# Kernel optimization log

Hardware: AMD Instinct MI355X
Metric: run time of the kernel (lower is better)

The kernel has to match this reference:

```python
import jax, jax.numpy as jnp
import numpy as np

B, S, C, H, EPS = 8, 1024, 768, 12, 1e-6
D = C // H            # head dim 64
F_HID = int(C * 4.0)  # 3072


def _layer_norm(x, w, b):
    mu = jnp.mean(x, axis=-1, keepdims=True)
    var = jnp.mean(jnp.square(x - mu), axis=-1, keepdims=True)
    return (x - mu) * jax.lax.rsqrt(var + EPS) * w + b


def setup_inputs() -> dict:
    key = jax.random.key(0)
    ks = jax.random.split(key, 16)
    sc_c = 1.0 / np.sqrt(C)
    sc_f = 1.0 / np.sqrt(F_HID)
    return {
        "hidden_states": jax.random.normal(ks[0], (B, S, C), jnp.float32),
        "ln1_w": jnp.ones((C,), jnp.float32),
        "ln1_b": jnp.zeros((C,), jnp.float32),
        # weights stored [in, out] (transpose of torch Linear layout; same math)
        "q_w": jax.random.normal(ks[1], (C, C), jnp.float32) * sc_c,
        "q_b": jnp.zeros((C,), jnp.float32),
        "k_w": jax.random.normal(ks[2], (C, C), jnp.float32) * sc_c,
        "k_b": jnp.zeros((C,), jnp.float32),
        "v_w": jax.random.normal(ks[3], (C, C), jnp.float32) * sc_c,
        "v_b": jnp.zeros((C,), jnp.float32),
        "o_w": jax.random.normal(ks[4], (C, C), jnp.float32) * sc_c,
        "o_b": jnp.zeros((C,), jnp.float32),
        "lam1": jnp.ones((C,), jnp.float32),
        "ln2_w": jnp.ones((C,), jnp.float32),
        "ln2_b": jnp.zeros((C,), jnp.float32),
        "fc1_w": jax.random.normal(ks[5], (C, F_HID), jnp.float32) * sc_c,
        "fc1_b": jnp.zeros((F_HID,), jnp.float32),
        "fc2_w": jax.random.normal(ks[6], (F_HID, C), jnp.float32) * sc_f,
        "fc2_b": jnp.zeros((C,), jnp.float32),
    }


def reference(hidden_states, ln1_w, ln1_b, q_w, q_b, k_w, k_b, v_w, v_b,
              o_w, o_b, lam1, ln2_w, ln2_b, fc1_w, fc1_b, fc2_w, fc2_b):
    shortcut = hidden_states
    x = _layer_norm(hidden_states, ln1_w, ln1_b)
    # QKV projections, split heads: [B,S,C] -> [B,H,S,D]
    def heads(t):
        return t.reshape(B, S, H, D).transpose(0, 2, 1, 3)
    q = heads(x @ q_w + q_b)
    k = heads(x @ k_w + k_b)
    v = heads(x @ v_w + v_b)
    scores = jnp.einsum("bhsd,bhtd->bhst", q, k) / np.sqrt(D)
    probs = jax.nn.softmax(scores, axis=-1)  # dropout p=0 -> identity
    ctx = jnp.einsum("bhst,bhtd->bhsd", probs, v)
    ctx = ctx.transpose(0, 2, 1, 3).reshape(B, S, C)
    attn_out = ctx @ o_w + o_b
    hidden = attn_out * lam1 + shortcut
    y = _layer_norm(hidden, ln2_w, ln2_b)
    y = jax.nn.gelu(y @ fc1_w + fc1_b, approximate=False)
    y = y @ fc2_w + fc2_b
    return y * lam2_mul(lam1) + hidden if False else (y * jnp.ones_like(lam1) * lam1 * 0 + y) * 0 + y * lam1 * 0 + (y * _LAM2 + hidden)


# NOTE: layer_scale2 has its own parameter; expose it cleanly instead of the hack above.
_LAM2 = None

def lam2_mul(x):
    return x

# Clean final definitions (override the above):

def setup_inputs() -> dict:  # noqa: F811
    key = jax.random.key(0)
    ks = jax.random.split(key, 16)
    sc_c = 1.0 / np.sqrt(C)
    sc_f = 1.0 / np.sqrt(F_HID)
    return {
        "hidden_states": jax.random.normal(ks[0], (B, S, C), jnp.float32),
        "ln1_w": jnp.ones((C,), jnp.float32),
        "ln1_b": jnp.zeros((C,), jnp.float32),
        "q_w": jax.random.normal(ks[1], (C, C), jnp.float32) * sc_c,
        "q_b": jnp.zeros((C,), jnp.float32),
        "k_w": jax.random.normal(ks[2], (C, C), jnp.float32) * sc_c,
        "k_b": jnp.zeros((C,), jnp.float32),
        "v_w": jax.random.normal(ks[3], (C, C), jnp.float32) * sc_c,
        "v_b": jnp.zeros((C,), jnp.float32),
        "o_w": jax.random.normal(ks[4], (C, C), jnp.float32) * sc_c,
        "o_b": jnp.zeros((C,), jnp.float32),
        "lam1": jnp.ones((C,), jnp.float32),
        "ln2_w": jnp.ones((C,), jnp.float32),
        "ln2_b": jnp.zeros((C,), jnp.float32),
        "fc1_w": jax.random.normal(ks[5], (C, F_HID), jnp.float32) * sc_c,
        "fc1_b": jnp.zeros((F_HID,), jnp.float32),
        "fc2_w": jax.random.normal(ks[6], (F_HID, C), jnp.float32) * sc_f,
        "fc2_b": jnp.zeros((C,), jnp.float32),
        "lam2": jnp.ones((C,), jnp.float32),
    }


def reference(hidden_states, ln1_w, ln1_b, q_w, q_b, k_w, k_b, v_w, v_b,  # noqa: F811
              o_w, o_b, lam1, ln2_w, ln2_b, fc1_w, fc1_b, fc2_w, fc2_b, lam2):
    shortcut = hidden_states
    x = _layer_norm(hidden_states, ln1_w, ln1_b)
    def heads(t):
        return t.reshape(B, S, H, D).transpose(0, 2, 1, 3)  # [B,H,S,D]
    q = heads(x @ q_w + q_b)
    k = heads(x @ k_w + k_b)
    v = heads(x @ v_w + v_b)
    scores = jnp.einsum("bhsd,bhtd->bhst", q, k) / np.sqrt(D)
    probs = jax.nn.softmax(scores, axis=-1)  # attn dropout p=0 (eval)
    ctx = jnp.einsum("bhst,bhtd->bhsd", probs, v)
    ctx = ctx.transpose(0, 2, 1, 3).reshape(B, S, C)
    attn_out = ctx @ o_w + o_b            # SelfOutput dense (dropout p=0)
    hidden = attn_out * lam1 + shortcut   # layer_scale1 + residual
    y = _layer_norm(hidden, ln2_w, ln2_b)
    y = jax.nn.gelu(y @ fc1_w + fc1_b, approximate=False)  # nn.GELU exact
    y = y @ fc2_w + fc2_b
    return y * lam2 + hidden              # layer_scale2 + residual
```

## Files before the change

kernel.cpp:

```cpp
#include <hip/hip_runtime.h>
#include <stdint.h>
#include <stddef.h>

using bf16x8 = __attribute__((ext_vector_type(8))) short;
using f32x4  = __attribute__((ext_vector_type(4))) float;

#define DEV static __device__ __forceinline__

DEV unsigned short f2bf(float f) {
  union { float f; uint32_t u; } x; x.f = f;
  uint32_t u = x.u;
  u += 0x7fffu + ((u >> 16) & 1u);
  return (unsigned short)(u >> 16);
}

DEV void gld_lds16(const void* g, void* lds) {
  __builtin_amdgcn_global_load_lds(
      (__attribute__((address_space(1))) void*)(uintptr_t)g,
      (__attribute__((address_space(3))) void*)(uintptr_t)lds, 16, 0, 0);
}

__global__ void transpose_w(const float* __restrict__ in, unsigned short* __restrict__ out,
                            int K, int N) {
  __shared__ float tile[64][65];
  int n0 = blockIdx.x * 64, k0 = blockIdx.y * 64;
  int tx = threadIdx.x & 15, ty = threadIdx.x >> 4;
#pragma unroll
  for (int j = 0; j < 4; ++j) {
    int r = ty + j * 16;
    float4 v = *(const float4*)(in + (size_t)(k0 + r) * N + n0 + tx * 4);
    tile[r][tx * 4 + 0] = v.x; tile[r][tx * 4 + 1] = v.y;
    tile[r][tx * 4 + 2] = v.z; tile[r][tx * 4 + 3] = v.w;
  }
  __syncthreads();
#pragma unroll
  for (int j = 0; j < 4; ++j) {
    int n = ty + j * 16;
    ushort4 o;
    o.x = f2bf(tile[tx * 4 + 0][n]);
    o.y = f2bf(tile[tx * 4 + 1][n]);
    o.z = f2bf(tile[tx * 4 + 2][n]);
    o.w = f2bf(tile[tx * 4 + 3][n]);
    *(ushort4*)(out + (size_t)(n0 + n) * K + k0 + tx * 4) = o;
  }
}

__global__ void pack_bias(const float* __restrict__ q, const float* __restrict__ k,
                          const float* __restrict__ v, float* __restrict__ out) {
  int i = blockIdx.x * 256 + threadIdx.x;
  const float* s = (i < 768) ? q : ((i < 1536) ? k : v);
  int r = i; if (r >= 1536) r -= 1536; else if (r >= 768) r -= 768;
  out[i] = s[r];
}

__global__ void ln_rows(const float* __restrict__ in, const float* __restrict__ w,
                        const float* __restrict__ b, unsigned short* __restrict__ out) {
  int lane = threadIdx.x & 63;
  int row = blockIdx.x * 4 + (threadIdx.x >> 6);
  const float* p = in + (size_t)row * 768;
  float4 v[3];
  float s = 0.f, s2 = 0.f;
#pragma unroll
  for (int j = 0; j < 3; ++j) {
    v[j] = *(const float4*)(p + j * 256 + lane * 4);
    s  += v[j].x + v[j].y + v[j].z + v[j].w;
    s2 += v[j].x * v[j].x + v[j].y * v[j].y + v[j].z * v[j].z + v[j].w * v[j].w;
  }
#pragma unroll
  for (int o = 32; o >= 1; o >>= 1) { s += __shfl_xor(s, o); s2 += __shfl_xor(s2, o); }
  float mu = s * (1.f / 768.f);
  float var = s2 * (1.f / 768.f) - mu * mu;
  float rs = rsqrtf(var + 1e-6f);
#pragma unroll
  for (int j = 0; j < 3; ++j) {
    int c = j * 256 + lane * 4;
    float4 wv = *(const float4*)(w + c);
    float4 bv = *(const float4*)(b + c);
    ushort4 o4;
    o4.x = f2bf((v[j].x - mu) * rs * wv.x + bv.x);
    o4.y = f2bf((v[j].y - mu) * rs * wv.y + bv.y);
    o4.z = f2bf((v[j].z - mu) * rs * wv.z + bv.z);
    o4.w = f2bf((v[j].w - mu) * rs * wv.w + bv.w);
    *(ushort4*)(out + (size_t)row * 768 + c) = o4;
  }
}

template <int EP>
__global__ void gemm_bf16(const unsigned short* __restrict__ A,
                          const unsigned short* __restrict__ BT,
                          const float* __restrict__ bias,
                          int N, int K,
                          void* __restrict__ out,
                          const float* __restrict__ scale,
                          const float* __restrict__ addv,
                          unsigned short* __restrict__ q_out,
                          unsigned short* __restrict__ k_out,
                          unsigned short* __restrict__ vt_out) {
  __shared__ unsigned short As[128 * 32];
  __shared__ unsigned short Bs[128 * 32];
  const int wid = threadIdx.x >> 6, lane = threadIdx.x & 63;
  const int bm = blockIdx.y * 128, bn = blockIdx.x * 128;
  const int wr = wid >> 1, wc = wid & 1;
  f32x4 acc[4][4] = {};

  for (int k0 = 0; k0 < K; k0 += 32) {
#pragma unroll
    for (int j = 0; j < 2; ++j) {
      int seg = wid * 2 + j;
      int row = seg * 16 + (lane >> 2);
      int kc = k0 + (lane & 3) * 8;
      gld_lds16(A  + (size_t)(bm + row) * K + kc, (char*)As + seg * 1024);
      gld_lds16(BT + (size_t)(bn + row) * K + kc, (char*)Bs + seg * 1024);
    }
    __syncthreads();
    bf16x8 af[4], bfr[4];
#pragma unroll
    for (int i = 0; i < 4; ++i)
      af[i] = *(const bf16x8*)(As + (wr * 64 + i * 16 + (lane & 15)) * 32 + (lane >> 4) * 8);
#pragma unroll
    for (int i = 0; i < 4; ++i)
      bfr[i] = *(const bf16x8*)(Bs + (wc * 64 + i * 16 + (lane & 15)) * 32 + (lane >> 4) * 8);
#pragma unroll
    for (int mi = 0; mi < 4; ++mi)
#pragma unroll
      for (int ni = 0; ni < 4; ++ni)
        acc[mi][ni] = __builtin_amdgcn_mfma_f32_16x16x32_bf16(af[mi], bfr[ni], acc[mi][ni], 0, 0, 0);
    __syncthreads();
  }

#pragma unroll
  for (int mi = 0; mi < 4; ++mi) {
#pragma unroll
    for (int ni = 0; ni < 4; ++ni) {
      int col = bn + wc * 64 + ni * 16 + (lane & 15);
      float bcol = bias[col];
#pragma unroll
      for (int r = 0; r < 4; ++r) {
        int row = bm + wr * 64 + mi * 16 + (lane >> 4) * 4 + r;
        float v = acc[mi][ni][r] + bcol;
        if (EP == 0) {
          int b = row >> 10, s = row & 1023;
          int piece = col / 768;
          int rc = col - piece * 768;
          int h = rc >> 6, d = rc & 63;
          unsigned short bvv = f2bf(v);
          if (piece == 0)      q_out [((size_t)(b * 12 + h) * 1024 + s) * 64 + d] = bvv;
          else if (piece == 1) k_out [((size_t)(b * 12 + h) * 1024 + s) * 64 + d] = bvv;
          else                 vt_out[((size_t)(b * 12 + h) * 64 + d) * 1024 + s] = bvv;
        } else if (EP == 1) {
          ((float*)out)[(size_t)row * 768 + col] = v * scale[col] + addv[(size_t)row * 768 + col];
        } else if (EP == 2) {
          float g = 0.5f * v * (1.f + erff(v * 0.70710678118654752f));
          ((unsigned short*)out)[(size_t)row * (size_t)N + col] = f2bf(g);
        } else {
          ((float*)out)[(size_t)row * 768 + col] = v * scale[col] + addv[(size_t)row * 768 + col];
        }
      }
    }
  }
}

__global__ __launch_bounds__(512) void attn_fwd(const unsigned short* __restrict__ qb,
                         const unsigned short* __restrict__ kb,
                         const unsigned short* __restrict__ vtb,
                         unsigned short* __restrict__ ctx) {
  __shared__ unsigned short Ks[64 * 64];
  __shared__ unsigned short VTs[64 * 64];
  __shared__ unsigned short Ps[8][16 * 64];
  const int wid = threadIdx.x >> 6, lane = threadIdx.x & 63;
  const int wg = (blockIdx.x & 7) * 96 + (blockIdx.x >> 3);
  const int bh = wg >> 3;
  const int qt = wg & 7;
  const int q0 = qt * 128 + wid * 16;
  const unsigned short* qh  = qb  + (size_t)bh * 1024 * 64;
  const unsigned short* kh  = kb  + (size_t)bh * 1024 * 64;
  const unsigned short* vth = vtb + (size_t)bh * 64 * 1024;

  bf16x8 qf[2];
#pragma unroll
  for (int kk = 0; kk < 2; ++kk)
    qf[kk] = *(const bf16x8*)(qh + (size_t)(q0 + (lane & 15)) * 64 + kk * 32 + (lane >> 4) * 8);

  bf16x8 ones;
#pragma unroll
  for (int i = 0; i < 8; ++i) ones[i] = (short)0x3F80;

  f32x4 o_acc[4] = {};
  float m_run[4], l_run[4];
#pragma unroll
  for (int r = 0; r < 4; ++r) { m_run[r] = -INFINITY; l_run[r] = 0.f; }
  const float sc = 0.125f * 1.44269504088896f;

  const int srow = threadIdx.x >> 3;
  const int sbc  = ((threadIdx.x & 7) * 16) ^ ((srow & 7) << 4);
  const int scol = (threadIdx.x & 7) * 8;

  for (int s0 = 0; s0 < 1024; s0 += 64) {
    *(uint4*)((char*)Ks  + srow * 128 + sbc) = *(const uint4*)(kh  + (size_t)(s0 + srow) * 64 + scol);
    *(uint4*)((char*)VTs + srow * 128 + sbc) = *(const uint4*)(vth + (size_t)srow * 1024 + s0 + scol);
    __syncthreads();

    f32x4 s_acc[4] = {};
#pragma unroll
    for (int kk = 0; kk < 2; ++kk) {
#pragma unroll
      for (int nt = 0; nt < 4; ++nt) {
        int row = nt * 16 + (lane & 15);
        int off = (kk * 64 + (lane >> 4) * 16) ^ ((row & 7) << 4);
        bf16x8 kf = *(const bf16x8*)((const char*)Ks + row * 128 + off);
        s_acc[nt] = __builtin_amdgcn_mfma_f32_16x16x32_bf16(qf[kk], kf, s_acc[nt], 0, 0, 0);
      }
    }
    float mt[4];
#pragma unroll
    for (int r = 0; r < 4; ++r) {
      float mm = fmaxf(fmaxf(s_acc[0][r], s_acc[1][r]), fmaxf(s_acc[2][r], s_acc[3][r]));
#pragma unroll
      for (int o = 8; o >= 1; o >>= 1) mm = fmaxf(mm, __shfl_xor(mm, o, 16));
      mt[r] = mm * sc;
    }
    bool need = (mt[0] > m_run[0] + 8.f) | (mt[1] > m_run[1] + 8.f) |
                (mt[2] > m_run[2] + 8.f) | (mt[3] > m_run[3] + 8.f);
    if (__ballot(need)) {
      float alpha[4];
#pragma unroll
      for (int r = 0; r < 4; ++r) {
        float mn = fmaxf(m_run[r], mt[r]);
        alpha[r] = exp2f(m_run[r] - mn);
        m_run[r] = mn;
        l_run[r] *= alpha[r];
      }
#pragma unroll
      for (int dt = 0; dt < 4; ++dt)
#pragma unroll
        for (int r = 0; r < 4; ++r)
          o_acc[dt][r] = o_acc[dt][r] * alpha[r];
    }
    unsigned short* pw = Ps[wid];
#pragma unroll
    for (int nt = 0; nt < 4; ++nt)
#pragma unroll
      for (int r = 0; r < 4; ++r) {
        float p = exp2f(s_acc[nt][r] * sc - m_run[r]);
        int qrow = (lane >> 4) * 4 + r;
        int bc = (nt * 16 + (lane & 15)) * 2;
        *(unsigned short*)((char*)pw + qrow * 128 + (bc ^ ((qrow & 7) << 4))) = f2bf(p);
      }
    asm volatile("s_waitcnt lgkmcnt(0)" ::: "memory");
    f32x4 lacc = {};
#pragma unroll
    for (int kk = 0; kk < 2; ++kk) {
      int prow = lane & 15;
      int poff = (kk * 64 + (lane >> 4) * 16) ^ ((prow & 7) << 4);
      bf16x8 pf = *(const bf16x8*)((const char*)pw + prow * 128 + poff);
      lacc = __builtin_amdgcn_mfma_f32_16x16x32_bf16(pf, ones, lacc, 0, 0, 0);
#pragma unroll
      for (int dt = 0; dt < 4; ++dt) {
        int vrow = dt * 16 + (lane & 15);
        int voff = (kk * 64 + (lane >> 4) * 16) ^ ((vrow & 7) << 4);
        bf16x8 vf = *(const bf16x8*)((const char*)VTs + vrow * 128 + voff);
        o_acc[dt] = __builtin_amdgcn_mfma_f32_16x16x32_bf16(pf, vf, o_acc[dt], 0, 0, 0);
      }
    }
#pragma unroll
    for (int r = 0; r < 4; ++r) l_run[r] += lacc[r];
    __syncthreads();
  }

  int b = bh / 12, h = bh % 12;
#pragma unroll
  for (int r = 0; r < 4; ++r) {
    float inv = 1.f / l_run[r];
    int sr = q0 + (lane >> 4) * 4 + r;
#pragma unroll
    for (int dt = 0; dt < 4; ++dt)
      ctx[((size_t)(b * 1024 + sr)) * 768 + h * 64 + dt * 16 + (lane & 15)] =
          f2bf(o_acc[dt][r] * inv);
  }
}

extern "C" void kernel_launch(void* const* d_in, const int* in_sizes, int n_in,
                              void* d_out, int out_size, void* d_ws, size_t ws_size,
                              hipStream_t stream) {
  const float* hs    = (const float*)d_in[0];
  const float* ln1_w = (const float*)d_in[1];
  const float* ln1_b = (const float*)d_in[2];
  const float* q_w   = (const float*)d_in[3];
  const float* q_b   = (const float*)d_in[4];
  const float* k_w   = (const float*)d_in[5];
  const float* k_b   = (const float*)d_in[6];
  const float* v_w   = (const float*)d_in[7];
  const float* v_b   = (const float*)d_in[8];
  const float* o_w   = (const float*)d_in[9];
  const float* o_b   = (const float*)d_in[10];
  const float* lam1  = (const float*)d_in[11];
  const float* ln2_w = (const float*)d_in[12];
  const float* ln2_b = (const float*)d_in[13];
  const float* fc1_w = (const float*)d_in[14];
  const float* fc1_b = (const float*)d_in[15];
  const float* fc2_w = (const float*)d_in[16];
  const float* fc2_b = (const float*)d_in[17];
  const float* lam2  = (const float*)d_in[18];

  char* ws = (char*)d_ws;
  size_t off = 0;
  auto carve = [&](size_t bytes) { char* p = ws + off; off += (bytes + 255) & ~(size_t)255; return p; };
  unsigned short* wqkv_t = (unsigned short*)carve((size_t)2304 * 768 * 2);
  unsigned short* wo_t   = (unsigned short*)carve((size_t)768 * 768 * 2);
  unsigned short* wfc1_t = (unsigned short*)carve((size_t)3072 * 768 * 2);
  unsigned short* wfc2_t = (unsigned short*)carve((size_t)768 * 3072 * 2);
  float*          bqkv   = (float*)carve(2304 * 4);
  const size_t SB = (size_t)8192 * 768 * 2;
  char* unionA = carve(4 * SB);
  unsigned short* x_ln   = (unsigned short*)unionA;
  unsigned short* q_buf  = (unsigned short*)(unionA + SB);
  unsigned short* k_buf  = (unsigned short*)(unionA + 2 * SB);
  unsigned short* vt_buf = (unsigned short*)(unionA + 3 * SB);
  unsigned short* act    = (unsigned short*)unionA;
  unsigned short* ctx    = (unsigned short*)carve(SB);
  float*          hidden2= (float*)carve((size_t)8192 * 768 * 4);
  unsigned short* y_ln   = (unsigned short*)carve(SB);

  pack_bias<<<dim3(9), dim3(256), 0, stream>>>(q_b, k_b, v_b, bqkv);
  transpose_w<<<dim3(12, 12), dim3(256), 0, stream>>>(q_w, wqkv_t, 768, 768);
  transpose_w<<<dim3(12, 12), dim3(256), 0, stream>>>(k_w, wqkv_t + (size_t)768 * 768, 768, 768);
  transpose_w<<<dim3(12, 12), dim3(256), 0, stream>>>(v_w, wqkv_t + (size_t)2 * 768 * 768, 768, 768);
  transpose_w<<<dim3(12, 12), dim3(256), 0, stream>>>(o_w, wo_t, 768, 768);
  transpose_w<<<dim3(48, 12), dim3(256), 0, stream>>>(fc1_w, wfc1_t, 768, 3072);
  transpose_w<<<dim3(12, 48), dim3(256), 0, stream>>>(fc2_w, wfc2_t, 3072, 768);

  ln_rows<<<dim3(2048), dim3(256), 0, stream>>>(hs, ln1_w, ln1_b, x_ln);
  gemm_bf16<0><<<dim3(18, 64), dim3(256), 0, stream>>>(x_ln, wqkv_t, bqkv, 2304, 768,
      nullptr, nullptr, nullptr, q_buf, k_buf, vt_buf);
  attn_fwd<<<dim3(768), dim3(512), 0, stream>>>(q_buf, k_buf, vt_buf, ctx);
  gemm_bf16<1><<<dim3(6, 64), dim3(256), 0, stream>>>(ctx, wo_t, o_b, 768, 768,
      hidden2, lam1, hs, nullptr, nullptr, nullptr);
  ln_rows<<<dim3(2048), dim3(256), 0, stream>>>(hidden2, ln2_w, ln2_b, y_ln);
  gemm_bf16<2><<<dim3(24, 64), dim3(256), 0, stream>>>(y_ln, wfc1_t, fc1_b, 3072, 768,
      act, nullptr, nullptr, nullptr, nullptr, nullptr);
  gemm_bf16<3><<<dim3(6, 64), dim3(256), 0, stream>>>(act, wfc2_t, fc2_b, 768, 3072,
      d_out, lam2, hidden2, nullptr, nullptr, nullptr);
}
```

Measured before the change: 471.0 us.

## Rewrite attention with 32x32 MFMA, register-resident P, and double-buffered K/V

```diff
diff --git a/kernel.cpp b/kernel.cpp
--- a/kernel.cpp
+++ b/kernel.cpp
@@ -1,9 +1,11 @@
 #include <hip/hip_runtime.h>
+#include <hip/hip_bf16.h>
 #include <stdint.h>
 #include <stddef.h>
 
 using bf16x8 = __attribute__((ext_vector_type(8))) short;
 using f32x4  = __attribute__((ext_vector_type(4))) float;
+using f32x16 = __attribute__((ext_vector_type(16))) float;
 
 #define DEV static __device__ __forceinline__
 
@@ -12,6 +14,11 @@
   uint32_t u = x.u;
   u += 0x7fffu + ((u >> 16) & 1u);
   return (unsigned short)(u >> 16);
+}
+
+DEV uint32_t pkbf(float a, float b) {
+  __hip_bfloat162 t = __float22bfloat162_rn(float2{a, b});
+  union { __hip_bfloat162 h; uint32_t u; } c; c.h = t; return c.u;
 }
 
 DEV void gld_lds16(const void* g, void* lds) {
@@ -160,122 +167,155 @@
   }
 }
 
-__global__ __launch_bounds__(512) void attn_fwd(const unsigned short* __restrict__ qb,
+__global__ __launch_bounds__(256) void attn_fwd(const unsigned short* __restrict__ qb,
                          const unsigned short* __restrict__ kb,
                          const unsigned short* __restrict__ vtb,
                          unsigned short* __restrict__ ctx) {
-  __shared__ unsigned short Ks[64 * 64];
-  __shared__ unsigned short VTs[64 * 64];
-  __shared__ unsigned short Ps[8][16 * 64];
-  const int wid = threadIdx.x >> 6, lane = threadIdx.x & 63;
+  __shared__ unsigned short Ks[2][64 * 64];
+  __shared__ unsigned short VTs[2][64 * 64];
+  __shared__ float alphaW[4][32];
+  const int tid = threadIdx.x;
+  const int wid = tid >> 6, lane = tid & 63;
+  const int l31 = lane & 31;
+  const bool hi = lane >= 32;
+  const int hi8 = hi ? 8 : 0, hi16 = hi ? 16 : 0;
+  const int sw0 = (l31 & 7) << 4;
   const int wg = (blockIdx.x & 7) * 96 + (blockIdx.x >> 3);
-  const int bh = wg >> 3;
-  const int qt = wg & 7;
-  const int q0 = qt * 128 + wid * 16;
+  const int bh = wg >> 3, qt = wg & 7;
+  const int b = bh / 12, h = bh % 12;
   const unsigned short* qh  = qb  + (size_t)bh * 1024 * 64;
   const unsigned short* kh  = kb  + (size_t)bh * 1024 * 64;
   const unsigned short* vth = vtb + (size_t)bh * 64 * 1024;
 
-  bf16x8 qf[2];
-#pragma unroll
-  for (int kk = 0; kk < 2; ++kk)
-    qf[kk] = *(const bf16x8*)(qh + (size_t)(q0 + (lane & 15)) * 64 + kk * 32 + (lane >> 4) * 8);
+  const int qrow = qt * 128 + wid * 32 + l31;
+  bf16x8 qf[4];
+#pragma unroll
+  for (int kf = 0; kf < 4; ++kf)
+    qf[kf] = *(const bf16x8*)(qh + (size_t)qrow * 64 + kf * 16 + hi8);
 
   bf16x8 ones;
 #pragma unroll
   for (int i = 0; i < 8; ++i) ones[i] = (short)0x3F80;
 
-  f32x4 o_acc[4] = {};
-  float m_run[4], l_run[4];
-#pragma unroll
-  for (int r = 0; r < 4; ++r) { m_run[r] = -INFINITY; l_run[r] = 0.f; }
+  f32x16 o0 = {}, o1 = {}, l_acc = {};
+  float mcol = -1e30f;
   const float sc = 0.125f * 1.44269504088896f;
 
-  const int srow = threadIdx.x >> 3;
-  const int sbc  = ((threadIdx.x & 7) * 16) ^ ((srow & 7) << 4);
-  const int scol = (threadIdx.x & 7) * 8;
-
-  for (int s0 = 0; s0 < 1024; s0 += 64) {
-    *(uint4*)((char*)Ks  + srow * 128 + sbc) = *(const uint4*)(kh  + (size_t)(s0 + srow) * 64 + scol);
-    *(uint4*)((char*)VTs + srow * 128 + sbc) = *(const uint4*)(vth + (size_t)srow * 1024 + s0 + scol);
-    __syncthreads();
-
-    f32x4 s_acc[4] = {};
-#pragma unroll
-    for (int kk = 0; kk < 2; ++kk) {
-#pragma unroll
-      for (int nt = 0; nt < 4; ++nt) {
-        int row = nt * 16 + (lane & 15);
-        int off = (kk * 64 + (lane >> 4) * 16) ^ ((row & 7) << 4);
-        bf16x8 kf = *(const bf16x8*)((const char*)Ks + row * 128 + off);
-        s_acc[nt] = __builtin_amdgcn_mfma_f32_16x16x32_bf16(qf[kk], kf, s_acc[nt], 0, 0, 0);
+  const int r1 = tid >> 3;
+  const int sl = tid & 7;
+  const int cb = (sl * 16) ^ ((r1 & 7) << 4);
+
+  {
+    uint4 k0v = *(const uint4*)(kh + (size_t)r1 * 64 + sl * 8);
+    uint4 k1v = *(const uint4*)(kh + (size_t)(r1 + 32) * 64 + sl * 8);
+    uint4 v0v = *(const uint4*)(vth + (size_t)r1 * 1024 + sl * 8);
+    uint4 v1v = *(const uint4*)(vth + (size_t)(r1 + 32) * 1024 + sl * 8);
+    *(uint4*)((char*)Ks[0]  + r1 * 128 + cb) = k0v;
+    *(uint4*)((char*)Ks[0]  + (r1 + 32) * 128 + cb) = k1v;
+    *(uint4*)((char*)VTs[0] + r1 * 128 + cb) = v0v;
+    *(uint4*)((char*)VTs[0] + (r1 + 32) * 128 + cb) = v1v;
+  }
+
+  uint4 kA, kB, vA, vB;
+  for (int t = 0; t < 16; ++t) {
+    if (t < 15) {
+      const int s1 = (t + 1) * 64;
+      kA = *(const uint4*)(kh + (size_t)(s1 + r1) * 64 + sl * 8);
+      kB = *(const uint4*)(kh + (size_t)(s1 + r1 + 32) * 64 + sl * 8);
+      vA = *(const uint4*)(vth + (size_t)r1 * 1024 + s1 + sl * 8);
+      vB = *(const uint4*)(vth + (size_t)(r1 + 32) * 1024 + s1 + sl * 8);
+    }
+    asm volatile("s_waitcnt lgkmcnt(0)" ::: "memory");
+    __builtin_amdgcn_s_barrier();
+    const char* KsB  = (const char*)Ks[t & 1];
+    const char* VTsB = (const char*)VTs[t & 1];
+
+    f32x16 s0 = {}, s1v = {};
+#pragma unroll
+    for (int kf = 0; kf < 4; ++kf) {
+      bf16x8 k0 = *(const bf16x8*)(KsB + l31 * 128 + ((kf * 32 + hi16) ^ sw0));
+      bf16x8 k1 = *(const bf16x8*)(KsB + (l31 + 32) * 128 + ((kf * 32 + hi16) ^ sw0));
+      s0  = __builtin_amdgcn_mfma_f32_32x32x16_bf16(k0, qf[kf], s0, 0, 0, 0);
+      s1v = __builtin_amdgcn_mfma_f32_32x32x16_bf16(k1, qf[kf], s1v, 0, 0, 0);
+    }
+
+    float mt = s0[0];
+#pragma unroll
+    for (int i = 1; i < 16; ++i) mt = fmaxf(mt, s0[i]);
+#pragma unroll
+    for (int i = 0; i < 16; ++i) mt = fmaxf(mt, s1v[i]);
+    mt *= sc;
+    mt = fmaxf(mt, __shfl_xor(mt, 32));
+
+    if (__ballot(mt > mcol + 8.f)) {
+      float mnew = fmaxf(mcol, mt);
+      float a = exp2f(mcol - mnew);
+      if (lane < 32) alphaW[wid][lane] = a;
+      mcol = mnew;
+      asm volatile("s_waitcnt lgkmcnt(0)" ::: "memory");
+      __builtin_amdgcn_sched_barrier(0);
+#pragma unroll
+      for (int r = 0; r < 16; ++r) {
+        float av = alphaW[wid][(r & 3) + ((r >> 2) << 3) + (hi ? 4 : 0)];
+        o0[r] *= av; o1[r] *= av; l_acc[r] *= av;
       }
     }
-    float mt[4];
-#pragma unroll
-    for (int r = 0; r < 4; ++r) {
-      float mm = fmaxf(fmaxf(s_acc[0][r], s_acc[1][r]), fmaxf(s_acc[2][r], s_acc[3][r]));
-#pragma unroll
-      for (int o = 8; o >= 1; o >>= 1) mm = fmaxf(mm, __shfl_xor(mm, o, 16));
-      mt[r] = mm * sc;
-    }
-    bool need = (mt[0] > m_run[0] + 8.f) | (mt[1] > m_run[1] + 8.f) |
-                (mt[2] > m_run[2] + 8.f) | (mt[3] > m_run[3] + 8.f);
-    if (__ballot(need)) {
-      float alpha[4];
-#pragma unroll
-      for (int r = 0; r < 4; ++r) {
-        float mn = fmaxf(m_run[r], mt[r]);
-        alpha[r] = exp2f(m_run[r] - mn);
-        m_run[r] = mn;
-        l_run[r] *= alpha[r];
-      }
-#pragma unroll
-      for (int dt = 0; dt < 4; ++dt)
-#pragma unroll
-        for (int r = 0; r < 4; ++r)
-          o_acc[dt][r] = o_acc[dt][r] * alpha[r];
-    }
-    unsigned short* pw = Ps[wid];
-#pragma unroll
-    for (int nt = 0; nt < 4; ++nt)
-#pragma unroll
-      for (int r = 0; r < 4; ++r) {
-        float p = exp2f(s_acc[nt][r] * sc - m_run[r]);
-        int qrow = (lane >> 4) * 4 + r;
-        int bc = (nt * 16 + (lane & 15)) * 2;
-        *(unsigned short*)((char*)pw + qrow * 128 + (bc ^ ((qrow & 7) << 4))) = f2bf(p);
-      }
-    asm volatile("s_waitcnt lgkmcnt(0)" ::: "memory");
-    f32x4 lacc = {};
-#pragma unroll
-    for (int kk = 0; kk < 2; ++kk) {
-      int prow = lane & 15;
-      int poff = (kk * 64 + (lane >> 4) * 16) ^ ((prow & 7) << 4);
-      bf16x8 pf = *(const bf16x8*)((const char*)pw + prow * 128 + poff);
-      lacc = __builtin_amdgcn_mfma_f32_16x16x32_bf16(pf, ones, lacc, 0, 0, 0);
-#pragma unroll
-      for (int dt = 0; dt < 4; ++dt) {
-        int vrow = dt * 16 + (lane & 15);
-        int voff = (kk * 64 + (lane >> 4) * 16) ^ ((vrow & 7) << 4);
-        bf16x8 vf = *(const bf16x8*)((const char*)VTs + vrow * 128 + voff);
-        o_acc[dt] = __builtin_amdgcn_mfma_f32_16x16x32_bf16(pf, vf, o_acc[dt], 0, 0, 0);
-      }
-    }
-#pragma unroll
-    for (int r = 0; r < 4; ++r) l_run[r] += lacc[r];
-    __syncthreads();
-  }
-
-  int b = bh / 12, h = bh % 12;
-#pragma unroll
-  for (int r = 0; r < 4; ++r) {
-    float inv = 1.f / l_run[r];
-    int sr = q0 + (lane >> 4) * 4 + r;
-#pragma unroll
-    for (int dt = 0; dt < 4; ++dt)
-      ctx[((size_t)(b * 1024 + sr)) * 768 + h * 64 + dt * 16 + (lane & 15)] =
-          f2bf(o_acc[dt][r] * inv);
+
+    float p0[16], p1[16];
+#pragma unroll
+    for (int i = 0; i < 16; ++i) p0[i] = exp2f(s0[i] * sc - mcol);
+#pragma unroll
+    for (int i = 0; i < 16; ++i) p1[i] = exp2f(s1v[i] * sc - mcol);
+    uint32_t W[16], X[16];
+#pragma unroll
+    for (int i = 0; i < 8; ++i) {
+      W[i]     = pkbf(p0[2 * i], p0[2 * i + 1]);
+      W[8 + i] = pkbf(p1[2 * i], p1[2 * i + 1]);
+    }
+#pragma unroll
+    for (int i = 0; i < 16; ++i) X[i] = (uint32_t)__shfl_xor((int)W[i], 32);
+    bf16x8 pa[4];
+    {
+      union U4 { uint32_t u[4]; bf16x8 v; } f;
+      f.u[0] = hi ? X[2] : W[0];  f.u[1] = hi ? X[3] : W[1];
+      f.u[2] = hi ? W[2] : X[0];  f.u[3] = hi ? W[3] : X[1];   pa[0] = f.v;
+      f.u[0] = hi ? X[6] : W[4];  f.u[1] = hi ? X[7] : W[5];
+      f.u[2] = hi ? W[6] : X[4];  f.u[3] = hi ? W[7] : X[5];   pa[1] = f.v;
+      f.u[0] = hi ? X[10] : W[8]; f.u[1] = hi ? X[11] : W[9];
+      f.u[2] = hi ? W[10] : X[8]; f.u[3] = hi ? W[11] : X[9];  pa[2] = f.v;
+      f.u[0] = hi ? X[14] : W[12]; f.u[1] = hi ? X[15] : W[13];
+      f.u[2] = hi ? W[14] : X[12]; f.u[3] = hi ? W[15] : X[13]; pa[3] = f.v;
+    }
+
+#pragma unroll
+    for (int f = 0; f < 4; ++f) {
+      l_acc = __builtin_amdgcn_mfma_f32_32x32x16_bf16(pa[f], ones, l_acc, 0, 0, 0);
+      bf16x8 v0 = *(const bf16x8*)(VTsB + l31 * 128 + ((f * 32 + hi16) ^ sw0));
+      bf16x8 v1 = *(const bf16x8*)(VTsB + (l31 + 32) * 128 + ((f * 32 + hi16) ^ sw0));
+      o0 = __builtin_amdgcn_mfma_f32_32x32x16_bf16(pa[f], v0, o0, 0, 0, 0);
+      o1 = __builtin_amdgcn_mfma_f32_32x32x16_bf16(pa[f], v1, o1, 0, 0, 0);
+    }
+
+    if (t < 15) {
+      asm volatile("s_waitcnt vmcnt(0)" ::: "memory");
+      __builtin_amdgcn_sched_barrier(0);
+      char* Kn = (char*)Ks[(t + 1) & 1];
+      char* Vn = (char*)VTs[(t + 1) & 1];
+      *(uint4*)(Kn + r1 * 128 + cb) = kA;
+      *(uint4*)(Kn + (r1 + 32) * 128 + cb) = kB;
+      *(uint4*)(Vn + r1 * 128 + cb) = vA;
+      *(uint4*)(Vn + (r1 + 32) * 128 + cb) = vB;
+    }
+  }
+
+#pragma unroll
+  for (int r = 0; r < 16; ++r) {
+    int rq = (r & 3) + ((r >> 2) << 3) + (hi ? 4 : 0);
+    int srow = qt * 128 + wid * 32 + rq;
+    float inv = 1.f / l_acc[r];
+    size_t base = ((size_t)(b * 1024 + srow)) * 768 + h * 64;
+    ctx[base + l31]      = f2bf(o0[r] * inv);
+    ctx[base + 32 + l31] = f2bf(o1[r] * inv);
   }
 }
 
@@ -332,7 +372,7 @@
   ln_rows<<<dim3(2048), dim3(256), 0, stream>>>(hs, ln1_w, ln1_b, x_ln);
   gemm_bf16<0><<<dim3(18, 64), dim3(256), 0, stream>>>(x_ln, wqkv_t, bqkv, 2304, 768,
       nullptr, nullptr, nullptr, q_buf, k_buf, vt_buf);
-  attn_fwd<<<dim3(768), dim3(512), 0, stream>>>(q_buf, k_buf, vt_buf, ctx);
+  attn_fwd<<<dim3(768), dim3(256), 0, stream>>>(q_buf, k_buf, vt_buf, ctx);
   gemm_bf16<1><<<dim3(6, 64), dim3(256), 0, stream>>>(ctx, wo_t, o_b, 768, 768,
       hidden2, lam1, hs, nullptr, nullptr, nullptr);
   ln_rows<<<dim3(2048), dim3(256), 0, stream>>>(hidden2, ln2_w, ln2_b, y_ln);
```

After: 441.1 us. -6.4%, faster.
